# Optimization experiments

Measured on AMD Instinct MI355X. Metric: run time of the kernel, lower is better.

The kernel has to match this reference:

```python
import jax, jax.numpy as jnp
import numpy as np

NEG_SLOPE = 0.2  # PyG GATConv default LeakyReLU slope


def gat_conv(x, src, dst, edge_attr, W, att_s, att_d, We, att_e, b, num_nodes):
    """PyG GATConv with heads=1, add_self_loops=False, edge_dim features."""
    h = x @ W                       # [N, d] shared lin for src/dst
    a_src = h @ att_s               # [N]
    a_dst = h @ att_d               # [N]
    a_edge = (edge_attr @ We) @ att_e  # [E]
    logits = jax.nn.leaky_relu(a_src[src] + a_dst[dst] + a_edge, NEG_SLOPE)  # [E]
    # segment softmax over edges sharing the same destination node
    seg_max = jax.ops.segment_max(logits, dst, num_segments=num_nodes)
    seg_max = jnp.where(jnp.isfinite(seg_max), seg_max, 0.0)
    num = jnp.exp(logits - seg_max[dst])
    den = jax.ops.segment_sum(num, dst, num_segments=num_nodes)
    alpha = num / (den[dst] + 1e-16)  # [E]
    out = jax.ops.segment_sum(alpha[:, None] * h[src], dst, num_segments=num_nodes)
    return out + b


def setup_inputs() -> dict:
    N, E, D = 50000, 800000, 64
    key = jax.random.key(0)
    ks = jax.random.split(key, 16)
    s = 1.0 / np.sqrt(D)
    inp = {
        "x": jax.random.normal(ks[0], (N, D), jnp.float32),
        "edge_index": jax.random.randint(ks[1], (2, E), 0, N, jnp.int32).astype(jnp.int64),
        "edge_attr": jax.random.uniform(ks[2], (E, 1), jnp.float32),
        # layer 1 params
        "W1": jax.random.normal(ks[3], (D, D), jnp.float32) * s,
        "att_s1": jax.random.normal(ks[4], (D,), jnp.float32) * s,
        "att_d1": jax.random.normal(ks[5], (D,), jnp.float32) * s,
        "We1": jax.random.normal(ks[6], (1, D), jnp.float32) * s,
        "att_e1": jax.random.normal(ks[7], (D,), jnp.float32) * s,
        "b1": jnp.zeros((D,), jnp.float32),
        # layer 2 params
        "W2": jax.random.normal(ks[8], (D, D), jnp.float32) * s,
        "att_s2": jax.random.normal(ks[9], (D,), jnp.float32) * s,
        "att_d2": jax.random.normal(ks[10], (D,), jnp.float32) * s,
        "We2": jax.random.normal(ks[11], (1, D), jnp.float32) * s,
        "att_e2": jax.random.normal(ks[12], (D,), jnp.float32) * s,
        "b2": jnp.zeros((D,), jnp.float32),
    }
    return inp


def reference(x, edge_index, edge_attr, W1, att_s1, att_d1, We1, att_e1, b1,
              W2, att_s2, att_d2, We2, att_e2, b2):
    N = x.shape[0]
    src, dst = edge_index[0], edge_index[1]
    h = gat_conv(x, src, dst, edge_attr, W1, att_s1, att_d1, We1, att_e1, b1, N)
    h = jax.nn.relu(h)  # dropout is identity in eval mode
    out = gat_conv(h, src, dst, edge_attr, W2, att_s2, att_d2, We2, att_e2, b2, N)
    return out
```

## Files before the change

### kernel.cpp

```cpp
#include <hip/hip_runtime.h>
#include <hip/hip_fp16.h>
#include <cstdint>

#define FEAT 64
#define NEG_SLOPE 0.2f
#define PBLK 128
#define NODE_SH 8
#define CAP 5120

__global__ void zero_prep_kernel(int* __restrict__ gcur,
                                 const float* __restrict__ We1, const float* __restrict__ ae1,
                                 const float* __restrict__ We2, const float* __restrict__ ae2,
                                 float* __restrict__ cbuf) {
    int tid = threadIdx.x;
    if (tid < 64) {
        for (int i = tid; i < 256; i += 64) gcur[i] = 0;
    } else if (tid < 192) {
        int lane = tid & 63;
        bool second = tid >= 128;
        const float* a = second ? We2 : We1;
        const float* b = second ? ae2 : ae1;
        float v = a[lane] * b[lane];
        #pragma unroll
        for (int off = 32; off; off >>= 1) v += __shfl_xor(v, off, 64);
        if (lane == 0) cbuf[second ? 1 : 0] = v;
    }
}

__global__ __launch_bounds__(256) void coarse_kernel(
        const int* __restrict__ src, const int* __restrict__ dst,
        const float* __restrict__ eattr, int* __restrict__ gcur,
        int2* __restrict__ tmp, int E) {
    __shared__ int lcnt[256];
    __shared__ int lcur[256];
    int p = blockIdx.x, tid = threadIdx.x;
    lcnt[tid] = 0;
    __syncthreads();
    int ch = (E + PBLK - 1) / PBLK;
    int beg = p * ch, end = min(E, beg + ch);
    for (int e = beg + tid; e < end; e += 256)
        atomicAdd(&lcnt[dst[e] >> NODE_SH], 1);
    __syncthreads();
    int c = lcnt[tid];
    lcur[tid] = c ? atomicAdd(&gcur[tid], c) : 0;
    __syncthreads();
    for (int e = beg + tid; e < end; e += 256) {
        int d = dst[e];
        int bkt = d >> NODE_SH;
        int slot = atomicAdd(&lcur[bkt], 1);
        tmp[(size_t)bkt * CAP + slot] =
            make_int2((int)(((unsigned)d << 16) | (unsigned)src[e]), __float_as_int(eattr[e]));
    }
}

__global__ __launch_bounds__(256) void fine_kernel(
        const int2* __restrict__ tmp, const int* __restrict__ gcur,
        int2* __restrict__ rowptr2, unsigned* __restrict__ epack, int N) {
    __shared__ int cnt[256];
    __shared__ int wsum[4];
    int b = blockIdx.x, tid = threadIdx.x;
    int base = b * CAP;
    int cb = gcur[b];
    cnt[tid] = 0;
    __syncthreads();
    for (int i = tid; i < cb; i += 256)
        atomicAdd(&cnt[((unsigned)tmp[base + i].x >> 16) & 255], 1);
    __syncthreads();
    int lane = tid & 63, wave = tid >> 6;
    int v = cnt[tid], orig = v;
    #pragma unroll
    for (int off = 1; off < 64; off <<= 1) {
        int t = __shfl_up(v, off, 64);
        if (lane >= off) v += t;
    }
    if (lane == 63) wsum[wave] = v;
    __syncthreads();
    int add = 0;
    for (int w = 0; w < wave; ++w) add += wsum[w];
    int excl = base + v + add - orig;
    int node = (b << NODE_SH) + tid;
    if (node < N) rowptr2[node] = make_int2(excl, excl + orig);
    __syncthreads();
    cnt[tid] = excl;
    __syncthreads();
    for (int i = tid; i < cb; i += 256) {
        int2 t2 = tmp[base + i];
        int d8 = ((unsigned)t2.x >> 16) & 255;
        int pos = atomicAdd(&cnt[d8], 1);
        unsigned packed = ((unsigned)t2.x << 16) |
                          (unsigned)__half_as_ushort(__float2half(__int_as_float(t2.y)));
        epack[pos] = packed;
    }
}

template <bool FP16_IN>
__global__ __launch_bounds__(256) void gemm_att_kernel(
        const void* __restrict__ Xv, const float* __restrict__ W,
        const float* __restrict__ att_s, const float* __restrict__ att_d,
        __half* __restrict__ Hh, float* __restrict__ a_src,
        float* __restrict__ a_dst, int N) {
    __shared__ float Ws[FEAT * FEAT];
    int tid = threadIdx.x, wave = tid >> 6, lane = tid & 63;

    const float4* W4 = (const float4*)W;
    float4* Ws4 = (float4*)Ws;
    #pragma unroll
    for (int i = 0; i < 4; ++i) Ws4[tid + i * 256] = W4[tid + i * 256];

    int row0 = blockIdx.x * 32 + wave * 8;
    float xv[8];
    #pragma unroll
    for (int r = 0; r < 8; ++r) {
        int row = row0 + r;
        float v = 0.f;
        if (row < N) {
            if constexpr (FP16_IN)
                v = __half2float(((const __half*)Xv)[(size_t)row * FEAT + lane]);
            else
                v = ((const float*)Xv)[(size_t)row * FEAT + lane];
        }
        xv[r] = v;
    }
    __syncthreads();

    float acc[8] = {0.f, 0.f, 0.f, 0.f, 0.f, 0.f, 0.f, 0.f};
    #pragma unroll
    for (int k = 0; k < FEAT; ++k) {
        float wk = Ws[k * FEAT + lane];
        #pragma unroll
        for (int r = 0; r < 8; ++r) {
            float xk = __uint_as_float(__builtin_amdgcn_readlane(__float_as_uint(xv[r]), k));
            acc[r] = fmaf(xk, wk, acc[r]);
        }
    }

    float as_w = att_s[lane], ad_w = att_d[lane];
    #pragma unroll
    for (int r = 0; r < 8; ++r) {
        int row = row0 + r;
        if (row >= N) break;
        Hh[(size_t)row * FEAT + lane] = __float2half(acc[r]);
        float sv = acc[r] * as_w;
        float dv = acc[r] * ad_w;
        #pragma unroll
        for (int off = 32; off; off >>= 1) {
            sv += __shfl_xor(sv, off, 64);
            dv += __shfl_xor(dv, off, 64);
        }
        if (lane == 0) { a_src[row] = sv; a_dst[row] = dv; }
    }
}

template <bool FINAL>
__global__ __launch_bounds__(256) void fused_agg_kernel(
        const int2* __restrict__ rowptr2, const unsigned* __restrict__ epack,
        const float* __restrict__ a_src, const float* __restrict__ a_dst,
        const float* __restrict__ cptr, const uint2* __restrict__ Hh2,
        const float* __restrict__ bias, void* __restrict__ OUTv, int N) {
    int tid = threadIdx.x;
    int wave = tid >> 6, lane = tid & 63;
    int grp = lane >> 4, gl = lane & 15;
    int grpBase = grp << 4;
    int node = blockIdx.x * 16 + wave * 4 + grp;
    bool valid = node < N;
    int2 be = valid ? rowptr2[node] : make_int2(0, 0);
    int beg = be.x, end = be.y;
    float c = *cptr;
    float adn = valid ? a_dst[node] : 0.f;

    float den = 0.f;
    float4 a0 = {0,0,0,0}, a1 = {0,0,0,0}, a2 = {0,0,0,0}, a3 = {0,0,0,0};

    int nchunk = (end - beg + 15) >> 4;
    int wc = nchunk;
    wc = max(wc, __shfl_xor(wc, 16, 64));
    wc = max(wc, __shfl_xor(wc, 32, 64));

    for (int ch = 0; ch < wc; ++ch) {
        int j = beg + ch * 16 + gl;
        int s = 0;
        float w = 0.f;
        if (j < end) {
            unsigned ep = epack[j];
            s = (int)(ep >> 16);
            float ea = __half2float(__ushort_as_half((unsigned short)(ep & 0xffffu)));
            float l = fmaf(c, ea, a_src[s] + adn);
            l = (l > 0.f) ? l : NEG_SLOPE * l;
            w = __expf(l);
        }
        den += w;

        #pragma unroll
        for (int half = 0; half < 2; ++half) {
            int kb = grpBase + half * 8;
            int   s0 = __shfl(s, kb + 0, 64), s1 = __shfl(s, kb + 1, 64);
            int   s2 = __shfl(s, kb + 2, 64), s3 = __shfl(s, kb + 3, 64);
            int   s4 = __shfl(s, kb + 4, 64), s5 = __shfl(s, kb + 5, 64);
            int   s6 = __shfl(s, kb + 6, 64), s7 = __shfl(s, kb + 7, 64);
            float w0 = __shfl(w, kb + 0, 64), w1 = __shfl(w, kb + 1, 64);
            float w2 = __shfl(w, kb + 2, 64), w3 = __shfl(w, kb + 3, 64);
            float w4 = __shfl(w, kb + 4, 64), w5 = __shfl(w, kb + 5, 64);
            float w6 = __shfl(w, kb + 6, 64), w7 = __shfl(w, kb + 7, 64);
            uint2 u0 = Hh2[(size_t)s0 * 16 + gl];
            uint2 u1 = Hh2[(size_t)s1 * 16 + gl];
            uint2 u2 = Hh2[(size_t)s2 * 16 + gl];
            uint2 u3 = Hh2[(size_t)s3 * 16 + gl];
            uint2 u4 = Hh2[(size_t)s4 * 16 + gl];
            uint2 u5 = Hh2[(size_t)s5 * 16 + gl];
            uint2 u6 = Hh2[(size_t)s6 * 16 + gl];
            uint2 u7 = Hh2[(size_t)s7 * 16 + gl];
            float2 f00 = __half22float2(*(__half2*)&u0.x), f01 = __half22float2(*(__half2*)&u0.y);
            float2 f10 = __half22float2(*(__half2*)&u1.x), f11 = __half22float2(*(__half2*)&u1.y);
            float2 f20 = __half22float2(*(__half2*)&u2.x), f21 = __half22float2(*(__half2*)&u2.y);
            float2 f30 = __half22float2(*(__half2*)&u3.x), f31 = __half22float2(*(__half2*)&u3.y);
            float2 f40 = __half22float2(*(__half2*)&u4.x), f41 = __half22float2(*(__half2*)&u4.y);
            float2 f50 = __half22float2(*(__half2*)&u5.x), f51 = __half22float2(*(__half2*)&u5.y);
            float2 f60 = __half22float2(*(__half2*)&u6.x), f61 = __half22float2(*(__half2*)&u6.y);
            float2 f70 = __half22float2(*(__half2*)&u7.x), f71 = __half22float2(*(__half2*)&u7.y);
            a0.x = fmaf(w0, f00.x, a0.x); a0.y = fmaf(w0, f00.y, a0.y);
            a0.z = fmaf(w0, f01.x, a0.z); a0.w = fmaf(w0, f01.y, a0.w);
            a1.x = fmaf(w1, f10.x, a1.x); a1.y = fmaf(w1, f10.y, a1.y);
            a1.z = fmaf(w1, f11.x, a1.z); a1.w = fmaf(w1, f11.y, a1.w);
            a2.x = fmaf(w2, f20.x, a2.x); a2.y = fmaf(w2, f20.y, a2.y);
            a2.z = fmaf(w2, f21.x, a2.z); a2.w = fmaf(w2, f21.y, a2.w);
            a3.x = fmaf(w3, f30.x, a3.x); a3.y = fmaf(w3, f30.y, a3.y);
            a3.z = fmaf(w3, f31.x, a3.z); a3.w = fmaf(w3, f31.y, a3.w);
            a0.x = fmaf(w4, f40.x, a0.x); a0.y = fmaf(w4, f40.y, a0.y);
            a0.z = fmaf(w4, f41.x, a0.z); a0.w = fmaf(w4, f41.y, a0.w);
            a1.x = fmaf(w5, f50.x, a1.x); a1.y = fmaf(w5, f50.y, a1.y);
            a1.z = fmaf(w5, f51.x, a1.z); a1.w = fmaf(w5, f51.y, a1.w);
            a2.x = fmaf(w6, f60.x, a2.x); a2.y = fmaf(w6, f60.y, a2.y);
            a2.z = fmaf(w6, f61.x, a2.z); a2.w = fmaf(w6, f61.y, a2.w);
            a3.x = fmaf(w7, f70.x, a3.x); a3.y = fmaf(w7, f70.y, a3.y);
            a3.z = fmaf(w7, f71.x, a3.z); a3.w = fmaf(w7, f71.y, a3.w);
        }
    }

    den += __shfl_xor(den, 1, 64);
    den += __shfl_xor(den, 2, 64);
    den += __shfl_xor(den, 4, 64);
    den += __shfl_xor(den, 8, 64);

    if (valid) {
        float4 b4 = ((const float4*)bias)[gl];
        float inv = 1.f / (den + 1e-16f);
        float ox = (a0.x + a1.x + a2.x + a3.x) * inv + b4.x;
        float oy = (a0.y + a1.y + a2.y + a3.y) * inv + b4.y;
        float oz = (a0.z + a1.z + a2.z + a3.z) * inv + b4.z;
        float ow = (a0.w + a1.w + a2.w + a3.w) * inv + b4.w;
        if constexpr (FINAL) {
            ((float4*)OUTv)[(size_t)node * 16 + gl] = make_float4(ox, oy, oz, ow);
        } else {
            __half2 h01 = __floats2half2_rn(fmaxf(ox, 0.f), fmaxf(oy, 0.f));
            __half2 h23 = __floats2half2_rn(fmaxf(oz, 0.f), fmaxf(ow, 0.f));
            uint2 u;
            u.x = *(unsigned*)&h01;
            u.y = *(unsigned*)&h23;
            ((uint2*)OUTv)[(size_t)node * 16 + gl] = u;
        }
    }
}


static inline size_t align256(size_t x) { return (x + 255) & ~size_t(255); }

extern "C" void kernel_launch(void* const* d_in, const int* in_sizes, int n_in,
                              void* d_out, int out_size, void* d_ws, size_t ws_size,
                              hipStream_t stream) {
    const float* x        = (const float*)d_in[0];
    const int*   eidx     = (const int*)d_in[1];
    const float* eattr    = (const float*)d_in[2];
    const float* W1       = (const float*)d_in[3];
    const float* att_s1   = (const float*)d_in[4];
    const float* att_d1   = (const float*)d_in[5];
    const float* We1      = (const float*)d_in[6];
    const float* att_e1   = (const float*)d_in[7];
    const float* b1       = (const float*)d_in[8];
    const float* W2       = (const float*)d_in[9];
    const float* att_s2   = (const float*)d_in[10];
    const float* att_d2   = (const float*)d_in[11];
    const float* We2      = (const float*)d_in[12];
    const float* att_e2   = (const float*)d_in[13];
    const float* b2       = (const float*)d_in[14];
    float* OUT = (float*)d_out;

    const int N = in_sizes[0] / FEAT;
    const int E = in_sizes[2];
    const int* src = eidx;
    const int* dst = eidx + E;
    const int NB = (N + (1 << NODE_SH) - 1) >> NODE_SH;

    char* ws = (char*)d_ws;
    size_t off = 0;
    __half* Hh     = (__half*)(ws + off); off = align256(off + (size_t)N * FEAT * 2);
    __half* out1h  = (__half*)(ws + off); off = align256(off + (size_t)N * FEAT * 2);
    float* a_src   = (float*)(ws + off); off = align256(off + (size_t)N * 4);
    float* a_dst   = (float*)(ws + off); off = align256(off + (size_t)N * 4);
    int2*  rowptr2 = (int2*)(ws + off); off = align256(off + (size_t)N * 8);
    int2*  tmp     = (int2*)(ws + off); off = align256(off + (size_t)NB * CAP * 8);
    unsigned* epack= (unsigned*)(ws + off); off = align256(off + (size_t)NB * CAP * 4);
    int*   gcur    = (int*)(ws + off); off = align256(off + 256 * 4);
    float* cbuf    = (float*)(ws + off); off = align256(off + 2 * 4);
    (void)ws_size;

    const int gemmBlocks = (N + 31) / 32;
    const int aggBlocks  = (N + 15) / 16;

    zero_prep_kernel<<<1, 256, 0, stream>>>(gcur, We1, att_e1, We2, att_e2, cbuf);
    coarse_kernel<<<PBLK, 256, 0, stream>>>(src, dst, eattr, gcur, tmp, E);
    fine_kernel<<<NB, 256, 0, stream>>>(tmp, gcur, rowptr2, epack, N);

    gemm_att_kernel<false><<<gemmBlocks, 256, 0, stream>>>(x, W1, att_s1, att_d1,
                                                           Hh, a_src, a_dst, N);
    fused_agg_kernel<false><<<aggBlocks, 256, 0, stream>>>(rowptr2, epack, a_src, a_dst,
                                                           cbuf + 0, (const uint2*)Hh, b1,
                                                           out1h, N);

    gemm_att_kernel<true><<<gemmBlocks, 256, 0, stream>>>(out1h, W2, att_s2, att_d2,
                                                          Hh, a_src, a_dst, N);
    fused_agg_kernel<true><<<aggBlocks, 256, 0, stream>>>(rowptr2, epack, a_src, a_dst,
                                                          cbuf + 1, (const uint2*)Hh, b2,
                                                          OUT, N);
}
```

Measured before the change: 156.1 us.

## Merge coarse edge bucketing with layer-1 GEMM into one heterogeneous launch

Fuses the coarse bucketing kernel and the first-layer GEMM/attention kernel into one launch. The first PBLK blocks do edge bucketing and the rest do the GEMM, so the two independent stages run side by side. This removes one launch and the serialization between them, and the few coarse blocks can hide behind GEMM work. Shared memory is reused between the two roles, and the split adds a branch plus possible load imbalance.

```diff
diff --git a/kernel.cpp b/kernel.cpp
--- a/kernel.cpp
+++ b/kernel.cpp
@@ -27,29 +27,82 @@
     }
 }
 
-__global__ __launch_bounds__(256) void coarse_kernel(
+__global__ __launch_bounds__(256) void coarse_gemm1_kernel(
         const int* __restrict__ src, const int* __restrict__ dst,
         const float* __restrict__ eattr, int* __restrict__ gcur,
-        int2* __restrict__ tmp, int E) {
-    __shared__ int lcnt[256];
-    __shared__ int lcur[256];
-    int p = blockIdx.x, tid = threadIdx.x;
-    lcnt[tid] = 0;
-    __syncthreads();
-    int ch = (E + PBLK - 1) / PBLK;
-    int beg = p * ch, end = min(E, beg + ch);
-    for (int e = beg + tid; e < end; e += 256)
-        atomicAdd(&lcnt[dst[e] >> NODE_SH], 1);
-    __syncthreads();
-    int c = lcnt[tid];
-    lcur[tid] = c ? atomicAdd(&gcur[tid], c) : 0;
-    __syncthreads();
-    for (int e = beg + tid; e < end; e += 256) {
-        int d = dst[e];
-        int bkt = d >> NODE_SH;
-        int slot = atomicAdd(&lcur[bkt], 1);
-        tmp[(size_t)bkt * CAP + slot] =
-            make_int2((int)(((unsigned)d << 16) | (unsigned)src[e]), __float_as_int(eattr[e]));
+        int2* __restrict__ tmp, int E,
+        const float* __restrict__ X, const float* __restrict__ W,
+        const float* __restrict__ att_s, const float* __restrict__ att_d,
+        __half* __restrict__ Hh, float* __restrict__ a_src,
+        float* __restrict__ a_dst, int N) {
+    __shared__ float smem[FEAT * FEAT];
+    int tid = threadIdx.x;
+
+    if (blockIdx.x < PBLK) {
+        int* lcnt = (int*)smem;
+        int* lcur = (int*)smem + 256;
+        int p = blockIdx.x;
+        lcnt[tid] = 0;
+        __syncthreads();
+        int ch = (E + PBLK - 1) / PBLK;
+        int beg = p * ch, end = min(E, beg + ch);
+        for (int e = beg + tid; e < end; e += 256)
+            atomicAdd(&lcnt[dst[e] >> NODE_SH], 1);
+        __syncthreads();
+        int c = lcnt[tid];
+        lcur[tid] = c ? atomicAdd(&gcur[tid], c) : 0;
+        __syncthreads();
+        for (int e = beg + tid; e < end; e += 256) {
+            int d = dst[e];
+            int bkt = d >> NODE_SH;
+            int slot = atomicAdd(&lcur[bkt], 1);
+            tmp[(size_t)bkt * CAP + slot] =
+                make_int2((int)(((unsigned)d << 16) | (unsigned)src[e]),
+                          __float_as_int(eattr[e]));
+        }
+        return;
+    }
+
+    int wave = tid >> 6, lane = tid & 63;
+    const float4* W4 = (const float4*)W;
+    float4* Ws4 = (float4*)smem;
+    #pragma unroll
+    for (int i = 0; i < 4; ++i) Ws4[tid + i * 256] = W4[tid + i * 256];
+
+    int row0 = (blockIdx.x - PBLK) * 32 + wave * 8;
+    float xv[8];
+    #pragma unroll
+    for (int r = 0; r < 8; ++r) {
+        int row = row0 + r;
+        xv[r] = (row < N) ? X[(size_t)row * FEAT + lane] : 0.f;
+    }
+    __syncthreads();
+
+    float acc[8] = {0.f, 0.f, 0.f, 0.f, 0.f, 0.f, 0.f, 0.f};
+    #pragma unroll
+    for (int k = 0; k < FEAT; ++k) {
+        float wk = smem[k * FEAT + lane];
+        #pragma unroll
+        for (int r = 0; r < 8; ++r) {
+            float xk = __uint_as_float(__builtin_amdgcn_readlane(__float_as_uint(xv[r]), k));
+            acc[r] = fmaf(xk, wk, acc[r]);
+        }
+    }
+
+    float as_w = att_s[lane], ad_w = att_d[lane];
+    #pragma unroll
+    for (int r = 0; r < 8; ++r) {
+        int row = row0 + r;
+        if (row >= N) break;
+        Hh[(size_t)row * FEAT + lane] = __float2half(acc[r]);
+        float sv = acc[r] * as_w;
+        float dv = acc[r] * ad_w;
+        #pragma unroll
+        for (int off = 32; off; off >>= 1) {
+            sv += __shfl_xor(sv, off, 64);
+            dv += __shfl_xor(dv, off, 64);
+        }
+        if (lane == 0) { a_src[row] = sv; a_dst[row] = dv; }
     }
 }
 
@@ -93,9 +146,8 @@
     }
 }
 
-template <bool FP16_IN>
-__global__ __launch_bounds__(256) void gemm_att_kernel(
-        const void* __restrict__ Xv, const float* __restrict__ W,
+__global__ __launch_bounds__(256) void gemm2_att_kernel(
+        const __half* __restrict__ Xh, const float* __restrict__ W,
         const float* __restrict__ att_s, const float* __restrict__ att_d,
         __half* __restrict__ Hh, float* __restrict__ a_src,
         float* __restrict__ a_dst, int N) {
@@ -112,14 +164,7 @@
     #pragma unroll
     for (int r = 0; r < 8; ++r) {
         int row = row0 + r;
-        float v = 0.f;
-        if (row < N) {
-            if constexpr (FP16_IN)
-                v = __half2float(((const __half*)Xv)[(size_t)row * FEAT + lane]);
-            else
-                v = ((const float*)Xv)[(size_t)row * FEAT + lane];
-        }
-        xv[r] = v;
+        xv[r] = (row < N) ? __half2float(Xh[(size_t)row * FEAT + lane]) : 0.f;
     }
     __syncthreads();
 
@@ -307,17 +352,19 @@
     const int aggBlocks  = (N + 15) / 16;
 
     zero_prep_kernel<<<1, 256, 0, stream>>>(gcur, We1, att_e1, We2, att_e2, cbuf);
-    coarse_kernel<<<PBLK, 256, 0, stream>>>(src, dst, eattr, gcur, tmp, E);
+
+    coarse_gemm1_kernel<<<PBLK + gemmBlocks, 256, 0, stream>>>(
+        src, dst, eattr, gcur, tmp, E,
+        x, W1, att_s1, att_d1, Hh, a_src, a_dst, N);
+
     fine_kernel<<<NB, 256, 0, stream>>>(tmp, gcur, rowptr2, epack, N);
 
-    gemm_att_kernel<false><<<gemmBlocks, 256, 0, stream>>>(x, W1, att_s1, att_d1,
-                                                           Hh, a_src, a_dst, N);
     fused_agg_kernel<false><<<aggBlocks, 256, 0, stream>>>(rowptr2, epack, a_src, a_dst,
                                                            cbuf + 0, (const uint2*)Hh, b1,
                                                            out1h, N);
 
-    gemm_att_kernel<true><<<gemmBlocks, 256, 0, stream>>>(out1h, W2, att_s2, att_d2,
-                                                          Hh, a_src, a_dst, N);
+    gemm2_att_kernel<<<gemmBlocks, 256, 0, stream>>>(out1h, W2, att_s2, att_d2,
+                                                     Hh, a_src, a_dst, N);
     fused_agg_kernel<true><<<aggBlocks, 256, 0, stream>>>(rowptr2, epack, a_src, a_dst,
                                                           cbuf + 1, (const uint2*)Hh, b2,
                                                           OUT, N);
```

Result: faster. 134.0 us, median of 2 (-14.1%).
